# Kernel optimization log

Measured on AMD Instinct MI355X. Metric: run time of the kernel, lower is better.

Reference implementation:

```python
import jax, jax.numpy as jnp
import numpy as np

BS, L, D = 2048, 32, 768
KS = 5  # gaussian kernel size
EPS = 1e-5


def layer_norm(x, g, b):
    m = x.mean(-1, keepdims=True)
    var = ((x - m) ** 2).mean(-1, keepdims=True)
    return (x - m) * jax.lax.rsqrt(var + EPS) * g + b


def setup_inputs() -> dict:
    key = jax.random.key(0)
    ks = jax.random.split(key, 12)
    s = 0.02
    return {
        "v": jax.random.normal(ks[0], (BS, L, D), jnp.float32),
        "qa": jax.random.normal(ks[1], (BS, D), jnp.float32),
        # v_proj: LayerNorm -> Linear(D,D) -> GELU
        "vp_lng": jnp.ones((D,), jnp.float32),
        "vp_lnb": jnp.zeros((D,), jnp.float32),
        "vp_w": jax.random.normal(ks[2], (D, D), jnp.float32) * s,
        "vp_b": jnp.zeros((D,), jnp.float32),
        # qa_proj: LayerNorm -> Linear(D,D) -> GELU
        "qp_lng": jnp.ones((D,), jnp.float32),
        "qp_lnb": jnp.zeros((D,), jnp.float32),
        "qp_w": jax.random.normal(ks[3], (D, D), jnp.float32) * s,
        "qp_b": jnp.zeros((D,), jnp.float32),
        # grounding: LayerNorm -> Linear(D,D/2) -> GELU -> Linear(D/2,1) -> Softmax(dim=-2)
        "g_lng": jnp.ones((D,), jnp.float32),
        "g_lnb": jnp.zeros((D,), jnp.float32),
        "g_w1": jax.random.normal(ks[4], (D, D // 2), jnp.float32) * s,
        "g_b1": jnp.zeros((D // 2,), jnp.float32),
        "g_w2": jax.random.normal(ks[5], (D // 2, 1), jnp.float32) * s,
        "g_b2": jnp.zeros((1,), jnp.float32),
        # adaptive gaussian filter sigma (scalar parameter, initial 1.0)
        "sigma": jnp.array(1.0, jnp.float32),
    }


def reference(v, qa, vp_lng, vp_lnb, vp_w, vp_b, qp_lng, qp_lnb, qp_w, qp_b,
              g_lng, g_lnb, g_w1, g_b1, g_w2, g_b2, sigma):
    bs, length = v.shape[0], v.shape[1]
    # projections (exact erf GELU, matching torch nn.GELU default)
    v_p = jax.nn.gelu(layer_norm(v, vp_lng, vp_lnb) @ vp_w + vp_b, approximate=False)
    qa_p = jax.nn.gelu(layer_norm(qa, qp_lng, qp_lnb) @ qp_w + qp_b, approximate=False)
    # gate = tanh(v @ qa) : [bs, L, 1]
    gate = jnp.tanh(jnp.einsum('bld,bd->bl', v_p, qa_p))[..., None]
    # grounding head -> softmax over frames
    h = layer_norm(v_p * gate, g_lng, g_lnb)
    h = jax.nn.gelu(h @ g_w1 + g_b1, approximate=False)
    logits = h @ g_w2 + g_b2                      # [bs, L, 1]
    ori_key = jax.nn.softmax(logits, axis=1)[..., 0]  # [bs, L]
    # adaptive gaussian smoothing (depthwise conv1d, symmetric 5-tap kernel) + softmax
    xk = jnp.arange(KS, dtype=jnp.float32) - KS // 2
    kern = jnp.exp(-0.5 * (xk / sigma) ** 2)
    kern = kern / kern.sum()
    xp = jnp.pad(ori_key, ((0, 0), (KS // 2, KS // 2)))
    taps = jnp.stack([xp[:, k:k + length] for k in range(KS)], axis=0)  # [KS, bs, L]
    smoothed = jnp.einsum('k,kbl->bl', kern, taps)
    key_gs = jax.nn.softmax(smoothed, axis=1)         # [bs, L]
    # find_best_interval_v2, vectorized: among windows of size {1,3,5} that
    # contain the (first) argmax frame, pick the window with highest prob-sum;
    # ties resolve to smallest window then earliest start (strict > in loop ==
    # first occurrence of the max in (w, start) order == jnp.argmax semantics).
    pmax = jnp.argmax(key_gs, axis=1)                 # [bs]
    cum = jnp.pad(jnp.cumsum(key_gs, axis=1), ((0, 0), (1, 0)))
    scores_all, starts_all, ends_all = [], [], []
    for w in (1, 3, 5):
        s = jnp.arange(length - w + 1)
        sums = cum[:, s + w] - cum[:, s]              # sliding window sums
        contains = (pmax[:, None] >= s[None, :]) & (pmax[:, None] < s[None, :] + w)
        scores_all.append(jnp.where(contains, sums, -jnp.inf))
        starts_all.append(s)
        ends_all.append(s + w)                        # NOTE: exclusive end stored, as in original
    scores = jnp.concatenate(scores_all, axis=1)
    starts = jnp.concatenate(starts_all)
    ends = jnp.concatenate(ends_all)
    idx = jnp.argmax(scores, axis=1)
    st = starts[idx]
    en = ends[idx]
    max_indices = jnp.stack([st, en], axis=1)         # [bs, 2]
    rng = jnp.arange(length)
    mask = (rng[None, :] >= st[:, None]) & (rng[None, :] <= en[:, None])
    start_time = st.astype(jnp.float32) / 31.0
    end_time = en.astype(jnp.float32) / 31.0
    return key_gs, max_indices, start_time, end_time, mask, ori_key
```

## Files before the change

### kernel.cpp

```cpp
#include <hip/hip_runtime.h>
#include <math.h>
#include <stdint.h>


#define DEV __device__ __forceinline__

typedef __attribute__((ext_vector_type(8))) short short8v;
typedef __attribute__((ext_vector_type(4))) float f32x4;

constexpr int KDIM  = 768;
constexpr int CHUNK = 32768;

constexpr int OFF_KG   = 0;
constexpr int OFF_MI   = 65536;
constexpr int OFF_ST   = 69632;
constexpr int OFF_ET   = 71680;
constexpr int OFF_MASK = 73728;
constexpr int OFF_ORI  = 139264;

DEV float wave_sum(float v) { for (int o = 32; o; o >>= 1) v += __shfl_xor(v, o); return v; }
DEV float wave_max(float v) { for (int o = 32; o; o >>= 1) v = fmaxf(v, __shfl_xor(v, o)); return v; }

DEV float gelu_fast(float x) {
    float z = x * 0.70710678118654752f;
    float s = fabsf(z);
    float t = __builtin_amdgcn_rcpf(fmaf(0.3275911f, s, 1.0f));
    float p = t * fmaf(t, fmaf(t, fmaf(t, fmaf(t, 1.061405429f, -1.453152027f),
                                       1.421413741f), -0.284496736f), 0.254829592f);
    float e = __expf(-s * s);
    float er = copysignf(1.0f - p * e, z);
    return 0.5f * x * (1.0f + er);
}

DEV short f2bf(float x) {
    uint32_t u = __builtin_bit_cast(uint32_t, x);
    u = u + 0x7fffu + ((u >> 16) & 1u);
    return (short)(u >> 16);
}
DEV float bf2f(short b) {
    uint32_t u = ((uint32_t)(uint16_t)b) << 16;
    return __builtin_bit_cast(float, u);
}
DEV float asf(uint32_t u) { return __builtin_bit_cast(float, u); }

DEV void gl_lds16(const void* g, void* l) {
    __builtin_amdgcn_global_load_lds(
        (const __attribute__((address_space(1))) uint32_t*)g,
        (__attribute__((address_space(3))) uint32_t*)l, 16, 0, 0);
}

__global__ __launch_bounds__(256)
void prep_A1(const float* __restrict__ X, const float* __restrict__ g,
             const float* __restrict__ b, short* __restrict__ Ah, short* __restrict__ Al)
{
    int w = threadIdx.x >> 6, lane = threadIdx.x & 63;
    int row = blockIdx.x * 4 + w;
    const float4* xr = (const float4*)(X + (size_t)row * KDIM);
    float4 xv[3]; float s = 0.f, ss = 0.f;
#pragma unroll
    for (int i = 0; i < 3; ++i) {
        xv[i] = xr[lane + i * 64];
        s  += xv[i].x + xv[i].y + xv[i].z + xv[i].w;
        ss += xv[i].x * xv[i].x + xv[i].y * xv[i].y + xv[i].z * xv[i].z + xv[i].w * xv[i].w;
    }
    s = wave_sum(s); ss = wave_sum(ss);
    float m = s * (1.f / 768.f), var = ss * (1.f / 768.f) - m * m;
    float sa = rsqrtf(var + 1e-5f), ta = -m * sa;
#pragma unroll
    for (int i = 0; i < 3; ++i) {
        int idx = lane + i * 64;
        float4 gv = ((const float4*)g)[idx];
        float4 bv = ((const float4*)b)[idx];
        float a0 = fmaf(fmaf(xv[i].x, sa, ta), gv.x, bv.x);
        float a1 = fmaf(fmaf(xv[i].y, sa, ta), gv.y, bv.y);
        float a2 = fmaf(fmaf(xv[i].z, sa, ta), gv.z, bv.z);
        float a3 = fmaf(fmaf(xv[i].w, sa, ta), gv.w, bv.w);
        short h0 = f2bf(a0), h1 = f2bf(a1), h2 = f2bf(a2), h3 = f2bf(a3);
        ushort4 hv, lv;
        hv.x = (uint16_t)h0; hv.y = (uint16_t)h1; hv.z = (uint16_t)h2; hv.w = (uint16_t)h3;
        lv.x = (uint16_t)f2bf(a0 - bf2f(h0)); lv.y = (uint16_t)f2bf(a1 - bf2f(h1));
        lv.z = (uint16_t)f2bf(a2 - bf2f(h2)); lv.w = (uint16_t)f2bf(a3 - bf2f(h3));
        ((ushort4*)(Ah + (size_t)row * KDIM))[idx] = hv;
        ((ushort4*)(Al + (size_t)row * KDIM))[idx] = lv;
    }
}

__global__ __launch_bounds__(256)
void prep_A2(const uint32_t* __restrict__ vp_hl, const float* __restrict__ qa_p,
             const float* __restrict__ g, const float* __restrict__ b,
             short* __restrict__ Ah, short* __restrict__ Al, int chunk_off)
{
    int w = threadIdx.x >> 6, lane = threadIdx.x & 63;
    int row = blockIdx.x * 4 + w;
    int bidx = (chunk_off + row) >> 5;
    const uint4*  hr = (const uint4*)(vp_hl + (size_t)row * KDIM);
    const float4* qr = (const float4*)(qa_p + (size_t)bidx * KDIM);
    float vp[12]; float s = 0.f, ss = 0.f, d = 0.f;
#pragma unroll
    for (int i = 0; i < 3; ++i) {
        uint4  uv = hr[lane + i * 64];
        float4 qv = qr[lane + i * 64];
        float v0 = asf(uv.x & 0xffff0000u) + asf(uv.x << 16);
        float v1 = asf(uv.y & 0xffff0000u) + asf(uv.y << 16);
        float v2 = asf(uv.z & 0xffff0000u) + asf(uv.z << 16);
        float v3 = asf(uv.w & 0xffff0000u) + asf(uv.w << 16);
        vp[i * 4 + 0] = v0; vp[i * 4 + 1] = v1; vp[i * 4 + 2] = v2; vp[i * 4 + 3] = v3;
        s  += v0 + v1 + v2 + v3;
        ss += v0 * v0 + v1 * v1 + v2 * v2 + v3 * v3;
        d  += v0 * qv.x + v1 * qv.y + v2 * qv.z + v3 * qv.w;
    }
    s = wave_sum(s); ss = wave_sum(ss); d = wave_sum(d);
    float gate = tanhf(d);
    float m = s * (1.f / 768.f), var = ss * (1.f / 768.f) - m * m;
    float den = rsqrtf(gate * gate * var + 1e-5f);
    float sa = gate * den, ta = -gate * m * den;
#pragma unroll
    for (int i = 0; i < 3; ++i) {
        int idx = lane + i * 64;
        float4 gv = ((const float4*)g)[idx];
        float4 bv = ((const float4*)b)[idx];
        float a0 = fmaf(fmaf(vp[i * 4 + 0], sa, ta), gv.x, bv.x);
        float a1 = fmaf(fmaf(vp[i * 4 + 1], sa, ta), gv.y, bv.y);
        float a2 = fmaf(fmaf(vp[i * 4 + 2], sa, ta), gv.z, bv.z);
        float a3 = fmaf(fmaf(vp[i * 4 + 3], sa, ta), gv.w, bv.w);
        short h0 = f2bf(a0), h1 = f2bf(a1), h2 = f2bf(a2), h3 = f2bf(a3);
        ushort4 hv, lv;
        hv.x = (uint16_t)h0; hv.y = (uint16_t)h1; hv.z = (uint16_t)h2; hv.w = (uint16_t)h3;
        lv.x = (uint16_t)f2bf(a0 - bf2f(h0)); lv.y = (uint16_t)f2bf(a1 - bf2f(h1));
        lv.z = (uint16_t)f2bf(a2 - bf2f(h2)); lv.w = (uint16_t)f2bf(a3 - bf2f(h3));
        ((ushort4*)(Ah + (size_t)row * KDIM))[idx] = hv;
        ((ushort4*)(Al + (size_t)row * KDIM))[idx] = lv;
    }
}

__global__ __launch_bounds__(256)
void prep_W(const float* __restrict__ W, short* __restrict__ Bh, short* __restrict__ Bl, int N)
{
    __shared__ float t[32][33];
    int bx = blockIdx.x, by = blockIdx.y;
    int lx = threadIdx.x & 31, ly = threadIdx.x >> 5;
#pragma unroll
    for (int r = 0; r < 32; r += 8)
        t[ly + r][lx] = W[(size_t)(by * 32 + ly + r) * N + bx * 32 + lx];
    __syncthreads();
#pragma unroll
    for (int r = 0; r < 32; r += 8) {
        float v = t[lx][ly + r];
        short hi = f2bf(v);
        size_t o = (size_t)(bx * 32 + ly + r) * KDIM + by * 32 + lx;
        Bh[o] = hi;
        Bl[o] = f2bf(v - bf2f(hi));
    }
}

#define VMW(N_) asm volatile("s_waitcnt vmcnt(" #N_ ")" ::: "memory")
#define SCB __builtin_amdgcn_sched_barrier(0)

#define STG(G_, KT_) gl_lds16(sp[G_] + (KT_) * 32,                            \
    lds + (((KT_) & 1) ? BUFSZ : 0) + (G_) * 4096 + toff)

#define STGA10(KT_) do { STG(0, KT_); STG(1, KT_); STG(2, KT_); STG(3, KT_);  \
    STG(4, KT_); STG(5, KT_); STG(6, KT_); STG(7, KT_); STG(8, KT_);          \
    STG(9, KT_); } while (0)

#define RDA(dst, BOFF) do { _Pragma("unroll")                                 \
    for (int mf = 0; mf < 4; ++mf) {                                          \
        int rA = wm * 64 + mf * 16 + lr;                                      \
        dst[mf] = *(const short8v*)(bb + (BOFF) + rA * 64 +                   \
                                    ((lh ^ ((rA >> 1) & 3)) << 4));           \
    } } while (0)

#define RDB(dst, BOFF) do { _Pragma("unroll")                                 \
    for (int nf = 0; nf < 6; ++nf) {                                          \
        int rB = wn * 96 + nf * 16 + lr;                                      \
        dst[nf] = *(const short8v*)(bb + (BOFF) + rB * 64 +                   \
                                    ((lh ^ ((rB >> 1) & 3)) << 4));           \
    } } while (0)

#define BODY(KT_, NL_) do {                                                   \
    if (NL_) { STGA10((KT_) + 1); }                                           \
    SCB;                                                                      \
    if (NL_) { VMW(10); } else { VMW(0); }                                    \
    SCB;                                                                      \
    __builtin_amdgcn_s_barrier();                \
    const char* bb = lds + (((KT_) & 1) ? BUFSZ : 0);                         \
    RDA(ah, 0); RDA(al, 8192); RDB(bh, 16384); RDB(bl, 28672);                \
    asm volatile("s_waitcnt lgkmcnt(0)" ::: "memory");                        \
    SCB;                                                                      \
    __builtin_amdgcn_s_barrier();                     \
    __builtin_amdgcn_s_setprio(1);                                            \
    _Pragma("unroll")                                                         \
    for (int mf = 0; mf < 4; ++mf)                                            \
        _Pragma("unroll")                                                     \
        for (int nf = 0; nf < 6; ++nf) {                                      \
            acc[mf][nf] = __builtin_amdgcn_mfma_f32_16x16x32_bf16(            \
                ah[mf], bh[nf], acc[mf][nf], 0, 0, 0);                        \
            acc[mf][nf] = __builtin_amdgcn_mfma_f32_16x16x32_bf16(            \
                ah[mf], bl[nf], acc[mf][nf], 0, 0, 0);                        \
            acc[mf][nf] = __builtin_amdgcn_mfma_f32_16x16x32_bf16(            \
                al[mf], bh[nf], acc[mf][nf], 0, 0, 0);                        \
        }                                                                     \
    __builtin_amdgcn_s_setprio(0);                                            \
    SCB;                                                                      \
} while (0)

template<int MODE>
__global__ __launch_bounds__(256, 2)
void gemm8(const short* __restrict__ Ah_g, const short* __restrict__ Al_g,
           const short* __restrict__ Bh_g, const short* __restrict__ Bl_g,
           const float* __restrict__ bias, uint32_t* __restrict__ O_hl,
           const float* __restrict__ w2, float* __restrict__ partials,
           int chunk_off)
{
    constexpr int BUFSZ = 40960;
    extern __shared__ __align__(16) char lds[];

    const int t = threadIdx.x;
    const int w = t >> 6, lane = t & 63;
    const int lr = lane & 15, lh = lane >> 4;
    const int wm = w >> 1, wn = w & 1;

    const int gx = gridDim.x, nwg = gx * gridDim.y;
    int bidx = blockIdx.y * gx + blockIdx.x;
    int wid = (bidx & 7) * (nwg >> 3) + (bidx >> 3);
    const int bx = wid % gx, by = wid / gx;
    const int row0 = by * 128, col0 = bx * 192;

    const int r_ = t >> 2, c_ = t & 3;
    const int swz_ = (c_ ^ ((r_ >> 1) & 3)) << 3;
    const int toff = t * 16;
    const short* sp[10];
    sp[0] = Ah_g + (size_t)(row0 + r_)       * KDIM + swz_;
    sp[1] = Ah_g + (size_t)(row0 + 64 + r_)  * KDIM + swz_;
    sp[2] = Al_g + (size_t)(row0 + r_)       * KDIM + swz_;
    sp[3] = Al_g + (size_t)(row0 + 64 + r_)  * KDIM + swz_;
    sp[4] = Bh_g + (size_t)(col0 + r_)       * KDIM + swz_;
    sp[5] = Bh_g + (size_t)(col0 + 64 + r_)  * KDIM + swz_;
    sp[6] = Bh_g + (size_t)(col0 + 128 + r_) * KDIM + swz_;
    sp[7] = Bl_g + (size_t)(col0 + r_)       * KDIM + swz_;
    sp[8] = Bl_g + (size_t)(col0 + 64 + r_)  * KDIM + swz_;
    sp[9] = Bl_g + (size_t)(col0 + 128 + r_) * KDIM + swz_;

    f32x4 acc[4][6] = {};
    short8v ah[4], al[4], bh[6], bl[6];

    STGA10(0);
    SCB;

    for (int kt = 0; kt < 24; kt += 2) {
        BODY(kt,     true);
        BODY(kt + 1, (kt + 1 < 23));
    }

    if (MODE == 0) {
#pragma unroll
        for (int mf = 0; mf < 4; ++mf)
#pragma unroll
            for (int nf = 0; nf < 6; ++nf) {
                int n = col0 + wn * 96 + nf * 16 + lr;
                float bvs = bias[n];
#pragma unroll
                for (int q = 0; q < 4; ++q) {
                    int m = row0 + wm * 64 + mf * 16 + lh * 4 + q;
                    float gv = gelu_fast(acc[mf][nf][q] + bvs);
                    uint32_t u  = __builtin_bit_cast(uint32_t, gv);
                    uint32_t hb = u & 0xffff0000u;
                    float rem   = gv - asf(hb);
                    O_hl[(size_t)m * 768 + n] =
                        hb | (uint32_t)(uint16_t)f2bf(rem);
                }
            }
    } else {
        float rs[4][4] = {};
#pragma unroll
        for (int mf = 0; mf < 4; ++mf)
#pragma unroll
            for (int nf = 0; nf < 6; ++nf) {
                int n = col0 + wn * 96 + nf * 16 + lr;
                float bvs = bias[n], wv = w2[n];
#pragma unroll
                for (int q = 0; q < 4; ++q)
                    rs[mf][q] += gelu_fast(acc[mf][nf][q] + bvs) * wv;
            }
#pragma unroll
        for (int mf = 0; mf < 4; ++mf)
#pragma unroll
            for (int q = 0; q < 4; ++q) {
                float vv = rs[mf][q];
                vv += __shfl_xor(vv, 1); vv += __shfl_xor(vv, 2);
                vv += __shfl_xor(vv, 4); vv += __shfl_xor(vv, 8);
                if (lr == 0) {
                    int m = chunk_off + row0 + wm * 64 + mf * 16 + lh * 4 + q;
                    partials[(size_t)(bx * 2 + wn) * 65536 + m] = vv;
                }
            }
    }
}

constexpr int BKF = 16;
__global__ __launch_bounds__(256)
void rowstats(const float* __restrict__ X, float2* __restrict__ st, int M)
{
    int wave = threadIdx.x >> 6, lane = threadIdx.x & 63;
    int row = blockIdx.x * 4 + wave;
    if (row >= M) return;
    const float4* xr = reinterpret_cast<const float4*>(X + (size_t)row * KDIM);
    float s = 0.f, ss = 0.f;
#pragma unroll
    for (int i = 0; i < 3; ++i) {
        float4 v = xr[lane + i * 64];
        s  += v.x + v.y + v.z + v.w;
        ss += v.x * v.x + v.y * v.y + v.z * v.z + v.w * v.w;
    }
    s = wave_sum(s); ss = wave_sum(ss);
    if (lane == 0) {
        float m = s * (1.0f / 768.0f);
        float var = ss * (1.0f / 768.0f) - m * m;
        float rstd = rsqrtf(var + 1e-5f);
        st[row] = make_float2(rstd, -m * rstd);
    }
}

template<int BM, int BN, int TM, int TN>
__global__ __launch_bounds__(256)
void gemm_fused(const float* __restrict__ X, const float2* __restrict__ st,
                const float* __restrict__ gw, const float* __restrict__ gb,
                const float* __restrict__ W, const float* __restrict__ bias,
                float* __restrict__ out, int M, int N)
{
    static_assert((BM / TM) * (BN / TN) == 256, "256 threads");
    __shared__ float As[BKF][BM];
    __shared__ float Bs[BKF][BN];
    const int t = threadIdx.x;
    constexpr int TXN = BN / TN;
    const int tx = t % TXN;
    const int ty = t / TXN;
    const int row0 = blockIdx.y * BM;
    const int col0 = blockIdx.x * BN;
    float acc[TM][TN] = {};
    constexpr int A_IT = BM * BKF / 4 / 256;
    constexpr int B_IT = BKF * BN / 4 / 256;
    for (int k0 = 0; k0 < KDIM; k0 += BKF) {
#pragma unroll
        for (int i = 0; i < A_IT; ++i) {
            int idx = t + i * 256;
            int r = idx >> 2;
            int c = (idx & 3) << 2;
            float4 xv = *reinterpret_cast<const float4*>(X + (size_t)(row0 + r) * KDIM + k0 + c);
            float2 s = st[row0 + r];
            float4 gv = *reinterpret_cast<const float4*>(gw + k0 + c);
            float4 bv = *reinterpret_cast<const float4*>(gb + k0 + c);
            As[c + 0][r] = fmaf(fmaf(xv.x, s.x, s.y), gv.x, bv.x);
            As[c + 1][r] = fmaf(fmaf(xv.y, s.x, s.y), gv.y, bv.y);
            As[c + 2][r] = fmaf(fmaf(xv.z, s.x, s.y), gv.z, bv.z);
            As[c + 3][r] = fmaf(fmaf(xv.w, s.x, s.y), gv.w, bv.w);
        }
#pragma unroll
        for (int i = 0; i < B_IT; ++i) {
            int idx = t + i * 256;
            int r = idx / (BN / 4);
            int c = (idx % (BN / 4)) << 2;
            *reinterpret_cast<float4*>(&Bs[r][c]) =
                *reinterpret_cast<const float4*>(W + (size_t)(k0 + r) * N + col0 + c);
        }
        __syncthreads();
#pragma unroll
        for (int kk = 0; kk < BKF; ++kk) {
            float a[TM], b[TN];
#pragma unroll
            for (int i = 0; i < TM; i += 4)
                *reinterpret_cast<float4*>(&a[i]) = *reinterpret_cast<const float4*>(&As[kk][ty * TM + i]);
#pragma unroll
            for (int j = 0; j < TN; j += 4)
                *reinterpret_cast<float4*>(&b[j]) = *reinterpret_cast<const float4*>(&Bs[kk][tx * TN + j]);
#pragma unroll
            for (int i = 0; i < TM; ++i)
#pragma unroll
                for (int j = 0; j < TN; ++j)
                    acc[i][j] = fmaf(a[i], b[j], acc[i][j]);
        }
        __syncthreads();
    }
#pragma unroll
    for (int i = 0; i < TM; ++i) {
        size_t row = row0 + ty * TM + i;
#pragma unroll
        for (int j = 0; j < TN; j += 4) {
            int col = col0 + tx * TN + j;
            float4 o;
            o.x = gelu_fast(acc[i][j + 0] + bias[col + 0]);
            o.y = gelu_fast(acc[i][j + 1] + bias[col + 1]);
            o.z = gelu_fast(acc[i][j + 2] + bias[col + 2]);
            o.w = gelu_fast(acc[i][j + 3] + bias[col + 3]);
            *reinterpret_cast<float4*>(out + row * N + col) = o;
        }
    }
}

__global__ __launch_bounds__(64)
void head_kernel(const float* __restrict__ partials, const float* __restrict__ b2,
                 const float* __restrict__ sigma_p, float* __restrict__ out)
{
    int b = blockIdx.x, lane = threadIdx.x;
    __shared__ float ok[36];
    __shared__ float kg[32];
    __shared__ int sel[2];

    if (lane < 36) ok[lane] = 0.f;
    __syncthreads();

    float x = -3.4e38f;
    if (lane < 32) {
        int row = b * 32 + lane;
        x = b2[0];
#pragma unroll
        for (int p = 0; p < 4; ++p) x += partials[(size_t)p * 65536 + row];
    }
    float mx = wave_max(x);
    float e = (lane < 32) ? expf(x - mx) : 0.f;
    float sum = wave_sum(e);
    float ori = e / sum;
    if (lane < 32) {
        out[OFF_ORI + b * 32 + lane] = ori;
        ok[lane + 2] = ori;
    }
    __syncthreads();

    float sg = sigma_p[0];
    float kern[5]; float ks = 0.f;
#pragma unroll
    for (int k = 0; k < 5; ++k) { float xx = (float)(k - 2) / sg; kern[k] = expf(-0.5f * xx * xx); ks += kern[k]; }
    float sm = -3.4e38f;
    if (lane < 32) {
        sm = 0.f;
#pragma unroll
        for (int k = 0; k < 5; ++k) sm += (kern[k] / ks) * ok[lane + k];
    }
    float mx2 = wave_max(sm);
    float e2 = (lane < 32) ? expf(sm - mx2) : 0.f;
    float sum2 = wave_sum(e2);
    float kgv = e2 / sum2;
    if (lane < 32) {
        out[OFF_KG + b * 32 + lane] = kgv;
        kg[lane] = kgv;
    }
    __syncthreads();

    if (lane == 0) {
        int pm = 0; float bv = kg[0];
        for (int i = 1; i < 32; ++i) if (kg[i] > bv) { bv = kg[i]; pm = i; }
        float cum[33]; cum[0] = 0.f;
        for (int i = 0; i < 32; ++i) cum[i + 1] = cum[i] + kg[i];
        float bs = -3.4e38f; int bst = 0, ben = 0;
        const int wsz[3] = {1, 3, 5};
        for (int wi = 0; wi < 3; ++wi) {
            int w = wsz[wi];
            for (int s = 0; s + w <= 32; ++s) {
                if (pm >= s && pm < s + w) {
                    float sc = cum[s + w] - cum[s];
                    if (sc > bs) { bs = sc; bst = s; ben = s + w; }
                }
            }
        }
        out[OFF_MI + b * 2 + 0] = (float)bst;
        out[OFF_MI + b * 2 + 1] = (float)ben;
        out[OFF_ST + b] = (float)bst / 31.0f;
        out[OFF_ET + b] = (float)ben / 31.0f;
        sel[0] = bst; sel[1] = ben;
    }
    __syncthreads();
    if (lane < 32)
        out[OFF_MASK + b * 32 + lane] = (lane >= sel[0] && lane <= sel[1]) ? 1.0f : 0.0f;
}

extern "C" void kernel_launch(void* const* d_in, const int* in_sizes, int n_in,
                              void* d_out, int out_size, void* d_ws, size_t ws_size,
                              hipStream_t stream)
{
    const float* v      = (const float*)d_in[0];
    const float* qa     = (const float*)d_in[1];
    const float* vp_lng = (const float*)d_in[2];
    const float* vp_lnb = (const float*)d_in[3];
    const float* vp_w   = (const float*)d_in[4];
    const float* vp_b   = (const float*)d_in[5];
    const float* qp_lng = (const float*)d_in[6];
    const float* qp_lnb = (const float*)d_in[7];
    const float* qp_w   = (const float*)d_in[8];
    const float* qp_b   = (const float*)d_in[9];
    const float* g_lng  = (const float*)d_in[10];
    const float* g_lnb  = (const float*)d_in[11];
    const float* g_w1   = (const float*)d_in[12];
    const float* g_b1   = (const float*)d_in[13];
    const float* g_w2   = (const float*)d_in[14];
    const float* g_b2   = (const float*)d_in[15];
    const float* sigma  = (const float*)d_in[16];
    float* outf = (float*)d_out;

    short* A1h = (short*)d_ws;
    short* A1l = A1h + (size_t)CHUNK * KDIM;
    uint32_t* vp_hl = (uint32_t*)(A1l + (size_t)CHUNK * KDIM);
    short* B1h = (short*)(vp_hl + (size_t)CHUNK * KDIM);
    short* B1l = B1h + 768 * KDIM;
    short* B2h = B1l + 768 * KDIM;
    short* B2l = B2h + 384 * KDIM;
    float* qa_p = (float*)(B2l + 384 * KDIM);
    float* st_qa = qa_p + 2048 * KDIM;
    float* partials = st_qa + 4096;

    rowstats<<<512, 256, 0, stream>>>(qa, (float2*)st_qa, 2048);
    gemm_fused<64, 64, 4, 4><<<dim3(12, 32), 256, 0, stream>>>(
        qa, (const float2*)st_qa, qp_lng, qp_lnb, qp_w, qp_b, qa_p, 2048, 768);

    prep_W<<<dim3(24, 24), 256, 0, stream>>>(vp_w, B1h, B1l, 768);
    prep_W<<<dim3(12, 24), 256, 0, stream>>>(g_w1, B2h, B2l, 384);

    constexpr int LDS8 = 81920;

    for (int c = 0; c < 65536; c += CHUNK) {
        prep_A1<<<CHUNK / 4, 256, 0, stream>>>(v + (size_t)c * KDIM, vp_lng, vp_lnb, A1h, A1l);
        gemm8<0><<<dim3(4, CHUNK / 128), 256, LDS8, stream>>>(
            A1h, A1l, B1h, B1l, vp_b, vp_hl, nullptr, nullptr, 0);
        prep_A2<<<CHUNK / 4, 256, 0, stream>>>(vp_hl, qa_p, g_lng, g_lnb, A1h, A1l, c);
        gemm8<1><<<dim3(2, CHUNK / 128), 256, LDS8, stream>>>(
            A1h, A1l, B2h, B2l, g_b1, nullptr, g_w2, partials, c);
    }

    head_kernel<<<2048, 64, 0, stream>>>(partials, g_b2, sigma, outf);
}
```

Before: 538.9 us.

## Fold gated LayerNorm into second GEMM epilogue and drop prep_A2 pass

Removes the prep_A2 pass that re-read the first GEMM's output to compute gate, mean and variance and write a normalized bf16 hi/lo copy. The first GEMM epilogue now writes split bf16 planes directly and emits per-row partial sums (sum, sum of squares, dot with qa_p). A small kernel turns these into per-row scale and shift, and the LayerNorm affine is folded algebraically: gamma is baked into W1 and column sums of W1 correct for mean and beta in the second GEMM epilogue. This saves a full read/write pass over the activations. In exchange it adds partial-sum traffic and feeds the unnormalized product into the GEMM, which may change precision.

```diff
diff --git a/kernel.cpp b/kernel.cpp
--- a/kernel.cpp
+++ b/kernel.cpp
@@ -86,55 +86,8 @@
 }
 
 __global__ __launch_bounds__(256)
-void prep_A2(const uint32_t* __restrict__ vp_hl, const float* __restrict__ qa_p,
-             const float* __restrict__ g, const float* __restrict__ b,
-             short* __restrict__ Ah, short* __restrict__ Al, int chunk_off)
-{
-    int w = threadIdx.x >> 6, lane = threadIdx.x & 63;
-    int row = blockIdx.x * 4 + w;
-    int bidx = (chunk_off + row) >> 5;
-    const uint4*  hr = (const uint4*)(vp_hl + (size_t)row * KDIM);
-    const float4* qr = (const float4*)(qa_p + (size_t)bidx * KDIM);
-    float vp[12]; float s = 0.f, ss = 0.f, d = 0.f;
-#pragma unroll
-    for (int i = 0; i < 3; ++i) {
-        uint4  uv = hr[lane + i * 64];
-        float4 qv = qr[lane + i * 64];
-        float v0 = asf(uv.x & 0xffff0000u) + asf(uv.x << 16);
-        float v1 = asf(uv.y & 0xffff0000u) + asf(uv.y << 16);
-        float v2 = asf(uv.z & 0xffff0000u) + asf(uv.z << 16);
-        float v3 = asf(uv.w & 0xffff0000u) + asf(uv.w << 16);
-        vp[i * 4 + 0] = v0; vp[i * 4 + 1] = v1; vp[i * 4 + 2] = v2; vp[i * 4 + 3] = v3;
-        s  += v0 + v1 + v2 + v3;
-        ss += v0 * v0 + v1 * v1 + v2 * v2 + v3 * v3;
-        d  += v0 * qv.x + v1 * qv.y + v2 * qv.z + v3 * qv.w;
-    }
-    s = wave_sum(s); ss = wave_sum(ss); d = wave_sum(d);
-    float gate = tanhf(d);
-    float m = s * (1.f / 768.f), var = ss * (1.f / 768.f) - m * m;
-    float den = rsqrtf(gate * gate * var + 1e-5f);
-    float sa = gate * den, ta = -gate * m * den;
-#pragma unroll
-    for (int i = 0; i < 3; ++i) {
-        int idx = lane + i * 64;
-        float4 gv = ((const float4*)g)[idx];
-        float4 bv = ((const float4*)b)[idx];
-        float a0 = fmaf(fmaf(vp[i * 4 + 0], sa, ta), gv.x, bv.x);
-        float a1 = fmaf(fmaf(vp[i * 4 + 1], sa, ta), gv.y, bv.y);
-        float a2 = fmaf(fmaf(vp[i * 4 + 2], sa, ta), gv.z, bv.z);
-        float a3 = fmaf(fmaf(vp[i * 4 + 3], sa, ta), gv.w, bv.w);
-        short h0 = f2bf(a0), h1 = f2bf(a1), h2 = f2bf(a2), h3 = f2bf(a3);
-        ushort4 hv, lv;
-        hv.x = (uint16_t)h0; hv.y = (uint16_t)h1; hv.z = (uint16_t)h2; hv.w = (uint16_t)h3;
-        lv.x = (uint16_t)f2bf(a0 - bf2f(h0)); lv.y = (uint16_t)f2bf(a1 - bf2f(h1));
-        lv.z = (uint16_t)f2bf(a2 - bf2f(h2)); lv.w = (uint16_t)f2bf(a3 - bf2f(h3));
-        ((ushort4*)(Ah + (size_t)row * KDIM))[idx] = hv;
-        ((ushort4*)(Al + (size_t)row * KDIM))[idx] = lv;
-    }
-}
-
-__global__ __launch_bounds__(256)
-void prep_W(const float* __restrict__ W, short* __restrict__ Bh, short* __restrict__ Bl, int N)
+void prep_W(const float* __restrict__ W, const float* __restrict__ scale,
+            short* __restrict__ Bh, short* __restrict__ Bl, int N)
 {
     __shared__ float t[32][33];
     int bx = blockIdx.x, by = blockIdx.y;
@@ -143,14 +96,49 @@
     for (int r = 0; r < 32; r += 8)
         t[ly + r][lx] = W[(size_t)(by * 32 + ly + r) * N + bx * 32 + lx];
     __syncthreads();
+    float sc = scale ? scale[by * 32 + lx] : 1.0f;
 #pragma unroll
     for (int r = 0; r < 32; r += 8) {
-        float v = t[lx][ly + r];
+        float v = t[lx][ly + r] * sc;
         short hi = f2bf(v);
         size_t o = (size_t)(bx * 32 + ly + r) * KDIM + by * 32 + lx;
         Bh[o] = hi;
         Bl[o] = f2bf(v - bf2f(hi));
     }
+}
+
+__global__ __launch_bounds__(256)
+void colsums(const float* __restrict__ W1, const float* __restrict__ g2,
+             const float* __restrict__ lb2, const float* __restrict__ b1,
+             float* __restrict__ c1, float* __restrict__ c2)
+{
+    int w = threadIdx.x >> 6, lane = threadIdx.x & 63;
+    int n = blockIdx.x * 4 + w;
+    float s1 = 0.f, s2 = 0.f;
+    for (int k = lane; k < 768; k += 64) {
+        float wv = W1[(size_t)k * 384 + n];
+        s1 += g2[k] * wv;
+        s2 += lb2[k] * wv;
+    }
+    s1 = wave_sum(s1); s2 = wave_sum(s2);
+    if (lane == 0) { c1[n] = s1; c2[n] = b1[n] + s2; }
+}
+
+__global__ __launch_bounds__(256)
+void stats2(const float* __restrict__ sums, float2* __restrict__ st2, int chunk_off)
+{
+    int r = chunk_off + blockIdx.x * 256 + threadIdx.x;
+    float s = 0.f, ss = 0.f, d = 0.f;
+#pragma unroll
+    for (int p = 0; p < 8; ++p) {
+        s  += sums[(size_t)(0 * 8 + p) * 65536 + r];
+        ss += sums[(size_t)(1 * 8 + p) * 65536 + r];
+        d  += sums[(size_t)(2 * 8 + p) * 65536 + r];
+    }
+    float gate = tanhf(d);
+    float m = s * (1.f / 768.f), var = ss * (1.f / 768.f) - m * m;
+    float den = rsqrtf(gate * gate * var + 1e-5f);
+    st2[r] = make_float2(gate * den, -gate * m * den);
 }
 
 #define VMW(N_) asm volatile("s_waitcnt vmcnt(" #N_ ")" ::: "memory")
@@ -208,9 +196,12 @@
 __global__ __launch_bounds__(256, 2)
 void gemm8(const short* __restrict__ Ah_g, const short* __restrict__ Al_g,
            const short* __restrict__ Bh_g, const short* __restrict__ Bl_g,
-           const float* __restrict__ bias, uint32_t* __restrict__ O_hl,
-           const float* __restrict__ w2, float* __restrict__ partials,
-           int chunk_off)
+           const float* __restrict__ bias,
+           short* __restrict__ Oh, short* __restrict__ Ol,
+           const float* __restrict__ qa_p, float* __restrict__ sums,
+           const float2* __restrict__ st2, const float* __restrict__ c1,
+           const float* __restrict__ c2, const float* __restrict__ w2,
+           float* __restrict__ partials, int chunk_off)
 {
     constexpr int BUFSZ = 40960;
     extern __shared__ __align__(16) char lds[];
@@ -253,34 +244,62 @@
     }
 
     if (MODE == 0) {
-#pragma unroll
-        for (int mf = 0; mf < 4; ++mf)
-#pragma unroll
-            for (int nf = 0; nf < 6; ++nf) {
-                int n = col0 + wn * 96 + nf * 16 + lr;
-                float bvs = bias[n];
-#pragma unroll
-                for (int q = 0; q < 4; ++q) {
-                    int m = row0 + wm * 64 + mf * 16 + lh * 4 + q;
-                    float gv = gelu_fast(acc[mf][nf][q] + bvs);
+        __syncthreads();
+        float* qal = (float*)lds;
+        int bbase = (chunk_off >> 5) + (row0 >> 5);
+        for (int j = t; j < 768; j += 256)
+            qal[j] = qa_p[(size_t)(bbase + j / 192) * 768 + col0 + (j % 192)];
+        __syncthreads();
+#pragma unroll
+        for (int mf = 0; mf < 4; ++mf) {
+            const int bp = wm * 2 + (mf >> 1);
+#pragma unroll
+            for (int q = 0; q < 4; ++q) {
+                int m = row0 + wm * 64 + mf * 16 + lh * 4 + q;
+                float s = 0.f, ssq = 0.f, d = 0.f;
+#pragma unroll
+                for (int nf = 0; nf < 6; ++nf) {
+                    int ncol = wn * 96 + nf * 16 + lr;
+                    int n = col0 + ncol;
+                    float gv = gelu_fast(acc[mf][nf][q] + bias[n]);
                     uint32_t u  = __builtin_bit_cast(uint32_t, gv);
                     uint32_t hb = u & 0xffff0000u;
                     float rem   = gv - asf(hb);
-                    O_hl[(size_t)m * 768 + n] =
-                        hb | (uint32_t)(uint16_t)f2bf(rem);
+                    Oh[(size_t)m * 768 + n] = (short)(hb >> 16);
+                    Ol[(size_t)m * 768 + n] = f2bf(rem);
+                    s += gv; ssq += gv * gv; d += gv * qal[bp * 192 + ncol];
+                }
+                for (int o = 1; o < 16; o <<= 1) {
+                    s += __shfl_xor(s, o); ssq += __shfl_xor(ssq, o); d += __shfl_xor(d, o);
+                }
+                if (lr == 0) {
+                    int gr = chunk_off + m;
+                    int pc = bx * 2 + wn;
+                    sums[(size_t)(0 * 8 + pc) * 65536 + gr] = s;
+                    sums[(size_t)(1 * 8 + pc) * 65536 + gr] = ssq;
+                    sums[(size_t)(2 * 8 + pc) * 65536 + gr] = d;
                 }
             }
+        }
     } else {
+        float c1v[6], c2v[6], wv[6];
+#pragma unroll
+        for (int nf = 0; nf < 6; ++nf) {
+            int n = col0 + wn * 96 + nf * 16 + lr;
+            c1v[nf] = c1[n]; c2v[nf] = c2[n]; wv[nf] = w2[n];
+        }
         float rs[4][4] = {};
 #pragma unroll
         for (int mf = 0; mf < 4; ++mf)
 #pragma unroll
-            for (int nf = 0; nf < 6; ++nf) {
-                int n = col0 + wn * 96 + nf * 16 + lr;
-                float bvs = bias[n], wv = w2[n];
-#pragma unroll
-                for (int q = 0; q < 4; ++q)
-                    rs[mf][q] += gelu_fast(acc[mf][nf][q] + bvs) * wv;
+            for (int q = 0; q < 4; ++q) {
+                int gm = chunk_off + row0 + wm * 64 + mf * 16 + lh * 4 + q;
+                float2 st = st2[gm];
+#pragma unroll
+                for (int nf = 0; nf < 6; ++nf) {
+                    float h = fmaf(st.x, acc[mf][nf][q], fmaf(st.y, c1v[nf], c2v[nf]));
+                    rs[mf][q] += gelu_fast(h) * wv[nf];
+                }
             }
 #pragma unroll
         for (int mf = 0; mf < 4; ++mf)
@@ -290,8 +309,8 @@
                 vv += __shfl_xor(vv, 1); vv += __shfl_xor(vv, 2);
                 vv += __shfl_xor(vv, 4); vv += __shfl_xor(vv, 8);
                 if (lr == 0) {
-                    int m = chunk_off + row0 + wm * 64 + mf * 16 + lh * 4 + q;
-                    partials[(size_t)(bx * 2 + wn) * 65536 + m] = vv;
+                    int gm = chunk_off + row0 + wm * 64 + mf * 16 + lh * 4 + q;
+                    partials[(size_t)(bx * 2 + wn) * 65536 + gm] = vv;
                 }
             }
     }
@@ -498,31 +517,39 @@
 
     short* A1h = (short*)d_ws;
     short* A1l = A1h + (size_t)CHUNK * KDIM;
-    uint32_t* vp_hl = (uint32_t*)(A1l + (size_t)CHUNK * KDIM);
-    short* B1h = (short*)(vp_hl + (size_t)CHUNK * KDIM);
+    short* vph = A1l + (size_t)CHUNK * KDIM;
+    short* vpl = vph + (size_t)CHUNK * KDIM;
+    short* B1h = vpl + (size_t)CHUNK * KDIM;
     short* B1l = B1h + 768 * KDIM;
     short* B2h = B1l + 768 * KDIM;
     short* B2l = B2h + 384 * KDIM;
     float* qa_p = (float*)(B2l + 384 * KDIM);
     float* st_qa = qa_p + 2048 * KDIM;
     float* partials = st_qa + 4096;
+    float* sums = partials + 4 * 65536;
+    float2* st2 = (float2*)(sums + 24 * 65536);
+    float* c1 = (float*)(st2 + 65536);
+    float* c2 = c1 + 384;
 
     rowstats<<<512, 256, 0, stream>>>(qa, (float2*)st_qa, 2048);
     gemm_fused<64, 64, 4, 4><<<dim3(12, 32), 256, 0, stream>>>(
         qa, (const float2*)st_qa, qp_lng, qp_lnb, qp_w, qp_b, qa_p, 2048, 768);
 
-    prep_W<<<dim3(24, 24), 256, 0, stream>>>(vp_w, B1h, B1l, 768);
-    prep_W<<<dim3(12, 24), 256, 0, stream>>>(g_w1, B2h, B2l, 384);
+    prep_W<<<dim3(24, 24), 256, 0, stream>>>(vp_w, nullptr, B1h, B1l, 768);
+    prep_W<<<dim3(12, 24), 256, 0, stream>>>(g_w1, g_lng, B2h, B2l, 384);
+    colsums<<<96, 256, 0, stream>>>(g_w1, g_lng, g_lnb, g_b1, c1, c2);
 
     constexpr int LDS8 = 81920;
 
     for (int c = 0; c < 65536; c += CHUNK) {
         prep_A1<<<CHUNK / 4, 256, 0, stream>>>(v + (size_t)c * KDIM, vp_lng, vp_lnb, A1h, A1l);
         gemm8<0><<<dim3(4, CHUNK / 128), 256, LDS8, stream>>>(
-            A1h, A1l, B1h, B1l, vp_b, vp_hl, nullptr, nullptr, 0);
-        prep_A2<<<CHUNK / 4, 256, 0, stream>>>(vp_hl, qa_p, g_lng, g_lnb, A1h, A1l, c);
+            A1h, A1l, B1h, B1l, vp_b, vph, vpl, qa_p, sums,
+            nullptr, nullptr, nullptr, nullptr, nullptr, c);
+        stats2<<<CHUNK / 256, 256, 0, stream>>>(sums, st2, c);
         gemm8<1><<<dim3(2, CHUNK / 128), 256, LDS8, stream>>>(
-            A1h, A1l, B2h, B2l, g_b1, nullptr, g_w2, partials, c);
+            vph, vpl, B2h, B2l, nullptr, nullptr, nullptr, nullptr, nullptr,
+            (const float2*)st2, c1, c2, g_w2, partials, c);
     }
 
     head_kernel<<<2048, 64, 0, stream>>>(partials, g_b2, sigma, outf);
```

Result: faster. 517.3 us (-4.0%).
